# Optimization experiments

Measured on AMD Instinct MI355X. Metric: run time of the kernel, lower is better.

Reference implementation:

```python
import jax, jax.numpy as jnp
import numpy as np

L, D, V = 8, 1024, 32000
DT_MIN, DT_MAX = 0.01, 0.1
EPS = 1e-5


def _layer_norm(x, w, b):
    mu = jnp.mean(x, -1, keepdims=True)
    var = jnp.var(x, -1, keepdims=True)
    return (x - mu) * jax.lax.rsqrt(var + EPS) * w + b


def _encode(ids):
    # deterministic phase encoding of tokens onto the unit phase sphere
    theta = 2.0 * jnp.pi * ids.astype(jnp.float32) / V  # [B,S]
    k = jnp.arange(1, D // 2 + 1, dtype=jnp.float32)
    ang = theta[..., None] * k  # [B,S,D/2]
    return jnp.concatenate([jnp.cos(ang), jnp.sin(ang)], -1) / jnp.sqrt(jnp.float32(D))


def _flux(s, mask):
    # attention-like causal score from state self-interaction
    score = jnp.einsum('bqd,bkd->bqk', s, s) / jnp.sqrt(jnp.float32(D))
    score = jnp.where(mask, score, 0.0)
    return jnp.einsum('bqk,bkd->bqd', score, s), score


def _evolve_with_tunneling(s, dt, mask):
    # Heun-Euler (predictor-corrector) integration step
    k1, score = _flux(s, mask)
    mid = s + dt * k1
    k2, _ = _flux(mid, mask)
    ev = s + 0.5 * dt * (k1 + k2)
    # quantum tunneling: boost low-energy states proportionally to dt/dt_max
    energy = jnp.linalg.norm(ev, axis=-1)  # [B,S]
    thr = jnp.mean(energy, axis=-1, keepdims=True)
    tunnel = energy < thr
    strength = dt / DT_MAX  # [B,1,1]
    ev = jnp.where(tunnel[..., None], ev * (1.0 + strength), ev)
    ratio = jnp.mean(tunnel.astype(jnp.float32))
    return ev, score, ratio


def setup_inputs() -> dict:
    key = jax.random.key(0)
    ks = jax.random.split(key, 4)
    B, S = 2, 2048
    input_ids = jax.random.randint(ks[0], (B, S), 0, V)
    labels = jax.random.randint(ks[1], (B, S), 0, V)
    proj_w = jax.random.normal(ks[2], (L, D, D), jnp.float32) * 0.02
    proj_b = jnp.zeros((L, D), jnp.float32)
    ln_w = jnp.ones((L, D), jnp.float32)
    ln_b = jnp.zeros((L, D), jnp.float32)
    fln_w = jnp.ones((D,), jnp.float32)
    fln_b = jnp.zeros((D,), jnp.float32)
    out_w = jax.random.normal(ks[3], (D, V), jnp.float32) * 0.02
    return dict(input_ids=input_ids, labels=labels, proj_w=proj_w, proj_b=proj_b,
                ln_w=ln_w, ln_b=ln_b, fln_w=fln_w, fln_b=fln_b, out_w=out_w)


def reference(input_ids, labels, proj_w, proj_b, ln_w, ln_b, fln_w, fln_b, out_w):
    B, S = input_ids.shape
    mask = jnp.tril(jnp.ones((S, S), dtype=bool))
    # deterministic timestep (midpoint of [dt_min, dt_max]); dropout in eval mode
    dt = jnp.full((B, 1, 1), 0.5 * (DT_MIN + DT_MAX), jnp.float32)
    states = _encode(input_ids)
    for i in range(L):
        ev, _score, _ratio = _evolve_with_tunneling(states, dt, mask)
        states = _layer_norm(ev @ proj_w[i] + proj_b[i], ln_w[i], ln_b[i])
    states = _layer_norm(states, fln_w, fln_b)
    # normalized quantum projection to vocab
    energy = jnp.linalg.norm(states, axis=-1, keepdims=True)
    logits = (states / (energy + 1e-12)) @ out_w  # [B,S,V]
    # shifted cross-entropy
    sl = logits[:, :-1, :].reshape(-1, V)
    tl = labels[:, 1:].reshape(-1)
    logp = jax.nn.log_softmax(sl, axis=-1)
    loss = -jnp.mean(jnp.take_along_axis(logp, tl[:, None], axis=1))
    return logits, loss
```

## Files before the change

### kernel.cpp

```cpp
#include <hip/hip_runtime.h>

#define LL 8
#define DD 1024
#define VV 32000
#define SS 2048
#define BB 2
#define NROWS 4096
#define DT_STEP 0.055f
#define HALF_DT 0.0275f
#define TUNNEL_SCALE 1.55f

typedef __attribute__((ext_vector_type(8))) short bf16x8;
typedef __attribute__((ext_vector_type(4))) float f32x4;

static __device__ __forceinline__ float bf2f(unsigned short u){
  union { unsigned int i; float f; } v; v.i = ((unsigned int)u) << 16; return v.f;
}
static __device__ __forceinline__ unsigned short f2bf(float f){
  union { float f; unsigned int i; } v; v.f = f;
  unsigned int r = v.i + 0x7fffu + ((v.i >> 16) & 1u);
  return (unsigned short)(r >> 16);
}

static __device__ __forceinline__ void gl16(const unsigned short* g, unsigned short* l){
  __builtin_amdgcn_global_load_lds(
      (const __attribute__((address_space(1))) unsigned int*)g,
      (__attribute__((address_space(3))) unsigned int*)l, 16, 0, 0);
}

__device__ __forceinline__ float block_sum256(float v, volatile float* scratch){
  #pragma unroll
  for (int off = 32; off; off >>= 1) v += __shfl_down(v, off, 64);
  int w = threadIdx.x >> 6, lane = threadIdx.x & 63;
  __syncthreads();
  if (lane == 0) scratch[w] = v;
  __syncthreads();
  return scratch[0] + scratch[1] + scratch[2] + scratch[3];
}

__global__ void encode_kernel(const int* __restrict__ ids, float* __restrict__ s_f32,
                              unsigned short* __restrict__ hi, unsigned short* __restrict__ lo){
  int row = blockIdx.x;
  int t = threadIdx.x;
  float theta = 6.28318530717958647692f * (float)ids[row] / 32000.0f;
  #pragma unroll
  for (int i = 0; i < 2; ++i){
    int kk = t + i * 256;
    float ang = theta * (float)(kk + 1);
    float sv, cv; sincosf(ang, &sv, &cv);
    float c = cv * 0.03125f, s = sv * 0.03125f;
    long b0 = (long)row * DD + kk, b1 = b0 + 512;
    s_f32[b0] = c; s_f32[b1] = s;
    unsigned short ch = f2bf(c); hi[b0] = ch; lo[b0] = f2bf(c - bf2f(ch));
    unsigned short sh = f2bf(s); hi[b1] = sh; lo[b1] = f2bf(s - bf2f(sh));
  }
}

__global__ void transpose_bf16_pair_kernel(const unsigned short* __restrict__ in_hi,
                                           const unsigned short* __restrict__ in_lo,
                                           unsigned short* __restrict__ out_hi,
                                           unsigned short* __restrict__ out_lo,
                                           int R, int C){
  __shared__ __align__(16) unsigned short tile[64][80];
  int zz = blockIdx.z;
  const unsigned short* in = (zz & 1) ? in_lo : in_hi;
  unsigned short* out = (zz & 1) ? out_lo : out_hi;
  long ib = (long)(zz >> 1) * R * C;
  int c0 = blockIdx.x * 64, r0 = blockIdx.y * 64;
  int t = threadIdx.x;
  #pragma unroll
  for (int i = 0; i < 2; ++i){
    int j = t + i * 256; int row = j >> 3, cc = j & 7;
    *(uint4*)&tile[row][cc * 8] = *(const uint4*)(in + ib + (long)(r0 + row) * C + c0 + cc * 8);
  }
  __syncthreads();
  #pragma unroll
  for (int i = 0; i < 2; ++i){
    int j = t + i * 256; int orow = j >> 3, cc = j & 7;
    union { unsigned short u[8]; uint4 v; } tmp;
    #pragma unroll
    for (int e = 0; e < 8; ++e) tmp.u[e] = tile[cc * 8 + e][orow];
    *(uint4*)(out + ib + (long)(c0 + orow) * R + r0 + cc * 8) = tmp.v;
  }
}

template<bool SPLIT>
__global__ void transpose_f32_bf16_kernel(const float* __restrict__ in,
                                          unsigned short* __restrict__ ohi,
                                          unsigned short* __restrict__ olo, int R, int C){
  __shared__ float tile[64][68];
  long ib = (long)blockIdx.z * R * C;
  int c0 = blockIdx.x * 64, r0 = blockIdx.y * 64;
  int t = threadIdx.x;
  #pragma unroll
  for (int i = 0; i < 4; ++i){
    int j = t + i * 256; int row = j >> 4, cc = j & 15;
    *(float4*)&tile[row][cc * 4] = *(const float4*)(in + ib + (long)(r0 + row) * C + c0 + cc * 4);
  }
  __syncthreads();
  #pragma unroll
  for (int i = 0; i < 2; ++i){
    int j = t + i * 256; int orow = j >> 3, cc = j & 7;
    union { unsigned short u[8]; uint4 v; } th, tl;
    #pragma unroll
    for (int e = 0; e < 8; ++e){
      float v = tile[cc * 8 + e][orow];
      unsigned short h = f2bf(v); th.u[e] = h;
      if (SPLIT) tl.u[e] = f2bf(v - bf2f(h));
    }
    long ob = ib + (long)(c0 + orow) * R + r0 + cc * 8;
    *(uint4*)(ohi + ob) = th.v;
    if (SPLIT) *(uint4*)(olo + ob) = tl.v;
  }
}

template<int OUTMODE, int CAUSAL>
__global__ __launch_bounds__(512, 4)
void gemm_nt_kernel(const unsigned short* __restrict__ Ahi, const unsigned short* __restrict__ Alo,
                    const unsigned short* __restrict__ Bhi, const unsigned short* __restrict__ Blo,
                    float* __restrict__ C, unsigned short* __restrict__ Chi,
                    unsigned short* __restrict__ Clo, const float* __restrict__ bias,
                    const float* __restrict__ Sf, const float* __restrict__ K1f,
                    int K, int lda, int ldb, int ldc, int MT, int NT,
                    long batchA, long batchB, long batchC, float alpha)
{
  const int bz = blockIdx.y;
  const int nwg = MT * NT;
  const int q = nwg >> 3, r = nwg & 7;
  const int xcd = blockIdx.x & 7, off = blockIdx.x >> 3;
  const int wg = (xcd < r ? xcd * (q + 1) : r * (q + 1) + (xcd - r) * q) + off;
  const int band = wg / (NT << 3), rem = wg - band * (NT << 3);
  const int mt = (band << 3) + (rem & 7), nt = rem >> 3;
  if (CAUSAL == 1 && nt > mt) return;
  const int m0 = mt << 7, n0 = nt << 7;
  int Keff = K;
  if (CAUSAL == 2){ int kl = (mt + 1) << 7; Keff = kl < K ? kl : K; }

  __shared__ __align__(16) unsigned short sA[2][128][64];
  __shared__ __align__(16) unsigned short sB[2][128][64];

  const int tid = threadIdx.x;
  const int lane = tid & 63;
  const int w = tid >> 6;
  const int wr = w >> 2, wc = w & 3;
  const int fr = lane & 15, fc = lane >> 4;
  const int fr7 = fr & 7;

  f32x4 acc[4][2];
  #pragma unroll
  for (int i = 0; i < 4; ++i)
    #pragma unroll
    for (int j = 0; j < 2; ++j) acc[i][j] = (f32x4){0.f, 0.f, 0.f, 0.f};

  const int srow = tid >> 3, slot = tid & 7;
  const int cont = slot ^ (srow & 7);
  const long aoff = (long)bz * batchA, boff = (long)bz * batchB;
  const int gcol = (cont & 3) << 3;
  const unsigned short* gA = (cont >= 4 ? Alo : Ahi) + aoff + (long)(m0 + srow) * lda + gcol;
  const unsigned short* gB = (cont >= 4 ? Blo : Bhi) + boff + (long)(n0 + srow) * ldb + gcol;
  const long rstepA = 64L * lda, rstepB = 64L * ldb;
  const int wofs = w << 9;

  #define STAGE(buf, kt) do {                                        \
    gl16(gA + (kt),          &sA[buf][0][0] + wofs);                 \
    gl16(gA + (kt) + rstepA, &sA[buf][0][0] + 4096 + wofs);          \
    gl16(gB + (kt),          &sB[buf][0][0] + wofs);                 \
    gl16(gB + (kt) + rstepB, &sB[buf][0][0] + 4096 + wofs);          \
  } while(0)

  const int oh = (fc ^ fr7) << 4;
  const int ol = ((4 + fc) ^ fr7) << 4;

  #define COMPUTE(buf) do {                                                         \
    const char* bA_ = (const char*)&sA[buf][0][0];                                  \
    const char* bB_ = (const char*)&sB[buf][0][0];                                  \
    bf16x8 ah_[4], al_[4];                                                          \
    _Pragma("unroll")                                                               \
    for (int mi = 0; mi < 4; ++mi){                                                 \
      const char* p_ = bA_ + (wr * 64 + mi * 16 + fr) * 128;                        \
      ah_[mi] = *(const bf16x8*)(p_ + oh);                                          \
      al_[mi] = *(const bf16x8*)(p_ + ol);                                          \
    }                                                                               \
    _Pragma("unroll")                                                               \
    for (int ni = 0; ni < 2; ++ni){                                                 \
      const char* pb_ = bB_ + (wc * 32 + ni * 16 + fr) * 128;                       \
      bf16x8 bh_ = *(const bf16x8*)(pb_ + oh);                                      \
      bf16x8 bl_ = *(const bf16x8*)(pb_ + ol);                                      \
      _Pragma("unroll")                                                             \
      for (int mi = 0; mi < 4; ++mi){                                               \
        acc[mi][ni] = __builtin_amdgcn_mfma_f32_16x16x32_bf16(ah_[mi], bh_, acc[mi][ni], 0, 0, 0);\
        acc[mi][ni] = __builtin_amdgcn_mfma_f32_16x16x32_bf16(ah_[mi], bl_, acc[mi][ni], 0, 0, 0);\
        acc[mi][ni] = __builtin_amdgcn_mfma_f32_16x16x32_bf16(al_[mi], bh_, acc[mi][ni], 0, 0, 0);\
      }                                                                             \
    }                                                                               \
  } while(0)

  const int ntiles = Keff >> 5;

  STAGE(0, 0);
  int cur = 0;
  for (int t = 0; t < ntiles - 1; ++t){
    asm volatile("s_barrier" ::: "memory");
    STAGE(cur ^ 1, (t + 1) << 5);
    asm volatile("s_waitcnt vmcnt(4)" ::: "memory");
    asm volatile("s_barrier" ::: "memory");
    COMPUTE(cur);
    cur ^= 1;
  }
  asm volatile("s_waitcnt vmcnt(0)" ::: "memory");
  asm volatile("s_barrier" ::: "memory");
  COMPUTE(cur);

  #undef STAGE
  #undef COMPUTE

  const long coff = (long)bz * batchC;
  const int rb0 = m0 + wr * 64 + fc * 4;
  const int cb0 = n0 + wc * 32 + fr;
  #pragma unroll
  for (int mi = 0; mi < 4; ++mi){
    #pragma unroll
    for (int ni = 0; ni < 2; ++ni){
      #pragma unroll
      for (int rg = 0; rg < 4; ++rg){
        int row = rb0 + mi * 16 + rg;
        int col = cb0 + ni * 16;
        float v = acc[mi][ni][rg] * alpha;
        long idx = coff + (long)row * ldc + col;
        if (OUTMODE == 0){
          if (bias) v += bias[col];
          C[idx] = v;
        } else if (OUTMODE == 2){
          if (CAUSAL == 1 && col > row) v = 0.0f;
          unsigned short h = f2bf(v);
          Chi[idx] = h;
          Clo[idx] = f2bf(v - bf2f(h));
        } else if (OUTMODE == 3){
          C[idx] = v;
          float m = Sf[idx] + DT_STEP * v;
          unsigned short h = f2bf(m);
          Chi[idx] = h;
          Clo[idx] = f2bf(m - bf2f(h));
        } else {
          C[idx] = Sf[idx] + HALF_DT * (K1f[idx] + v);
        }
      }
    }
  }
}

__global__ __launch_bounds__(512, 2)
void gemm256_kernel(const unsigned short* __restrict__ A,
                    const unsigned short* __restrict__ Bt,
                    float* __restrict__ C)
{
  const int MT = 16, NT = 125;
  const int nwg = MT * NT;
  const int q = nwg >> 3, r = nwg & 7;
  const int xcd = blockIdx.x & 7, off = blockIdx.x >> 3;
  const int wg = (xcd < r ? xcd * (q + 1) : r * (q + 1) + (xcd - r) * q) + off;
  const int band = wg / (NT << 3), rem = wg - band * (NT << 3);
  const int mt = (band << 3) + (rem & 7), nt = rem >> 3;
  const int m0 = mt << 8, n0 = nt << 8;

  __shared__ __align__(16) unsigned short sA[2][256][64];
  __shared__ __align__(16) unsigned short sB[2][256][64];

  const int tid = threadIdx.x;
  const int lane = tid & 63;
  const int w = tid >> 6;
  const int wr = w >> 2, wc = w & 3;
  const int fr = lane & 15, fc = lane >> 4;
  const int fr7 = fr & 7;

  f32x4 acc[8][4];
  #pragma unroll
  for (int i = 0; i < 8; ++i)
    #pragma unroll
    for (int j = 0; j < 4; ++j) acc[i][j] = (f32x4){0.f, 0.f, 0.f, 0.f};

  const int srow = tid >> 3, slot = tid & 7;
  const int cont = slot ^ (srow & 7);
  const unsigned short* gA = A  + (long)(m0 + srow) * DD + (cont << 3);
  const unsigned short* gB = Bt + (long)(n0 + srow) * DD + (cont << 3);
  const int wofs = w << 9;

  #define SGA(buf, kt, i) gl16(gA + (long)((i) * 64) * DD + (kt), &sA[buf][0][0] + (i) * 4096 + wofs)
  #define SGB(buf, kt, i) gl16(gB + (long)((i) * 64) * DD + (kt), &sB[buf][0][0] + (i) * 4096 + wofs)

  const int oh = (fc ^ fr7) << 4;
  const int ol = ((4 + fc) ^ fr7) << 4;

  #pragma unroll
  for (int i = 0; i < 4; ++i){ SGA(0, 0, i); SGB(0, 0, i); }

  int cur = 0;
  for (int t = 0; t < 16; ++t){
    const int nk = (t + 1) << 6;
    const bool stg = (t < 15);
    const char* bA = (const char*)&sA[cur][0][0];
    const char* bB = (const char*)&sB[cur][0][0];
    bf16x8 aq[4][2], bq[4][2];

    if (stg){ SGA(cur ^ 1, nk, 0); SGA(cur ^ 1, nk, 1);
              asm volatile("s_waitcnt vmcnt(2)" ::: "memory"); }
    else    { asm volatile("s_waitcnt vmcnt(0)" ::: "memory"); }
    asm volatile("s_barrier" ::: "memory");
    #pragma unroll
    for (int mi = 0; mi < 4; ++mi){
      const char* p = bA + (wr * 128 + mi * 16 + fr) * 128;
      aq[mi][0] = *(const bf16x8*)(p + oh);
      aq[mi][1] = *(const bf16x8*)(p + ol);
    }
    #pragma unroll
    for (int ni = 0; ni < 2; ++ni){
      const char* p = bB + (wc * 64 + ni * 16 + fr) * 128;
      bq[ni][0] = *(const bf16x8*)(p + oh);
      bq[ni][1] = *(const bf16x8*)(p + ol);
    }
    __builtin_amdgcn_s_setprio(1);
    #pragma unroll
    for (int ks = 0; ks < 2; ++ks)
      #pragma unroll
      for (int mi = 0; mi < 4; ++mi)
        #pragma unroll
        for (int ni = 0; ni < 2; ++ni)
          acc[mi][ni] = __builtin_amdgcn_mfma_f32_16x16x32_bf16(aq[mi][ks], bq[ni][ks], acc[mi][ni], 0, 0, 0);
    __builtin_amdgcn_s_setprio(0);

    if (stg){ SGA(cur ^ 1, nk, 2); SGA(cur ^ 1, nk, 3); }
    asm volatile("s_barrier" ::: "memory");
    #pragma unroll
    for (int ni = 2; ni < 4; ++ni){
      const char* p = bB + (wc * 64 + ni * 16 + fr) * 128;
      bq[ni][0] = *(const bf16x8*)(p + oh);
      bq[ni][1] = *(const bf16x8*)(p + ol);
    }
    __builtin_amdgcn_s_setprio(1);
    #pragma unroll
    for (int ks = 0; ks < 2; ++ks)
      #pragma unroll
      for (int mi = 0; mi < 4; ++mi)
        #pragma unroll
        for (int ni = 2; ni < 4; ++ni)
          acc[mi][ni] = __builtin_amdgcn_mfma_f32_16x16x32_bf16(aq[mi][ks], bq[ni][ks], acc[mi][ni], 0, 0, 0);
    __builtin_amdgcn_s_setprio(0);

    if (stg){ SGB(cur ^ 1, nk, 0); SGB(cur ^ 1, nk, 1); }
    asm volatile("s_barrier" ::: "memory");
    #pragma unroll
    for (int mi = 0; mi < 4; ++mi){
      const char* p = bA + (wr * 128 + (mi + 4) * 16 + fr) * 128;
      aq[mi][0] = *(const bf16x8*)(p + oh);
      aq[mi][1] = *(const bf16x8*)(p + ol);
    }
    __builtin_amdgcn_s_setprio(1);
    #pragma unroll
    for (int ks = 0; ks < 2; ++ks)
      #pragma unroll
      for (int mi = 0; mi < 4; ++mi)
        #pragma unroll
        for (int ni = 2; ni < 4; ++ni)
          acc[mi + 4][ni] = __builtin_amdgcn_mfma_f32_16x16x32_bf16(aq[mi][ks], bq[ni][ks], acc[mi + 4][ni], 0, 0, 0);
    __builtin_amdgcn_s_setprio(0);

    if (stg){ SGB(cur ^ 1, nk, 2); SGB(cur ^ 1, nk, 3); }
    asm volatile("s_barrier" ::: "memory");
    __builtin_amdgcn_s_setprio(1);
    #pragma unroll
    for (int ks = 0; ks < 2; ++ks)
      #pragma unroll
      for (int mi = 0; mi < 4; ++mi)
        #pragma unroll
        for (int ni = 0; ni < 2; ++ni)
          acc[mi + 4][ni] = __builtin_amdgcn_mfma_f32_16x16x32_bf16(aq[mi][ks], bq[ni][ks], acc[mi + 4][ni], 0, 0, 0);
    __builtin_amdgcn_s_setprio(0);

    cur ^= 1;
  }
  #undef SGA
  #undef SGB

  const int rb0 = m0 + wr * 128 + fc * 4;
  const int cb0 = n0 + wc * 64 + fr;
  #pragma unroll
  for (int mi = 0; mi < 8; ++mi){
    #pragma unroll
    for (int ni = 0; ni < 4; ++ni){
      #pragma unroll
      for (int rg = 0; rg < 4; ++rg){
        int row = rb0 + mi * 16 + rg;
        int col = cb0 + ni * 16;
        C[(long)row * VV + col] = acc[mi][ni][rg];
      }
    }
  }
}

__global__ void energy_kernel(const float* __restrict__ ev, float* __restrict__ energy){
  int row = blockIdx.x, t = threadIdx.x;
  long base = (long)row * DD + t * 4;
  float4 v = *(const float4*)(ev + base);
  __shared__ float scratch[4];
  float n2 = block_sum256(v.x*v.x + v.y*v.y + v.z*v.z + v.w*v.w, scratch);
  if (t == 0) energy[row] = sqrtf(n2);
}

__global__ void mean_energy_kernel(const float* __restrict__ energy, float* __restrict__ thr){
  int b = blockIdx.x, t = threadIdx.x;
  float s = 0.f;
  for (int j = t; j < SS; j += 256) s += energy[b * SS + j];
  __shared__ float scratch[4];
  float tot = block_sum256(s, scratch);
  if (t == 0) thr[b] = tot * (1.0f / SS);
}

__global__ void tunnel_kernel(const float* __restrict__ ev, const float* __restrict__ energy,
                              const float* __restrict__ thr,
                              unsigned short* __restrict__ hi, unsigned short* __restrict__ lo){
  int row = blockIdx.x, t = threadIdx.x;
  float scale = (energy[row] < thr[row >> 11]) ? TUNNEL_SCALE : 1.0f;
  long base = (long)row * DD + t * 4;
  float4 v = *(const float4*)(ev + base);
  v.x *= scale; v.y *= scale; v.z *= scale; v.w *= scale;
  ushort4 hv, lv;
  hv.x = f2bf(v.x); lv.x = f2bf(v.x - bf2f(hv.x));
  hv.y = f2bf(v.y); lv.y = f2bf(v.y - bf2f(hv.y));
  hv.z = f2bf(v.z); lv.z = f2bf(v.z - bf2f(hv.z));
  hv.w = f2bf(v.w); lv.w = f2bf(v.w - bf2f(hv.w));
  *(ushort4*)(hi + base) = hv; *(ushort4*)(lo + base) = lv;
}

__global__ void ln_kernel(const float* __restrict__ h, const float* __restrict__ w,
                          const float* __restrict__ b, float* __restrict__ s_f32,
                          unsigned short* __restrict__ hi, unsigned short* __restrict__ lo){
  int row = blockIdx.x, t = threadIdx.x;
  long base = (long)row * DD + t * 4;
  float4 xv = *(const float4*)(h + base);
  __shared__ float scratch[4];
  float sum = block_sum256(xv.x + xv.y + xv.z + xv.w, scratch);
  float ssq = block_sum256(xv.x*xv.x + xv.y*xv.y + xv.z*xv.z + xv.w*xv.w, scratch);
  float mu = sum * (1.0f / DD);
  float var = ssq * (1.0f / DD) - mu * mu;
  float rstd = rsqrtf(var + 1e-5f);
  float4 wv = *(const float4*)(w + t * 4), bv = *(const float4*)(b + t * 4);
  float y0 = (xv.x - mu) * rstd * wv.x + bv.x;
  float y1 = (xv.y - mu) * rstd * wv.y + bv.y;
  float y2 = (xv.z - mu) * rstd * wv.z + bv.z;
  float y3 = (xv.w - mu) * rstd * wv.w + bv.w;
  float4 o; o.x = y0; o.y = y1; o.z = y2; o.w = y3;
  *(float4*)(s_f32 + base) = o;
  ushort4 hv, lv;
  hv.x = f2bf(y0); lv.x = f2bf(y0 - bf2f(hv.x));
  hv.y = f2bf(y1); lv.y = f2bf(y1 - bf2f(hv.y));
  hv.z = f2bf(y2); lv.z = f2bf(y2 - bf2f(hv.z));
  hv.w = f2bf(y3); lv.w = f2bf(y3 - bf2f(hv.w));
  *(ushort4*)(hi + base) = hv; *(ushort4*)(lo + base) = lv;
}

__global__ void fln_kernel(const float* __restrict__ s, const float* __restrict__ w,
                           const float* __restrict__ b, unsigned short* __restrict__ uhi){
  int row = blockIdx.x, t = threadIdx.x;
  long base = (long)row * DD + t * 4;
  float4 xv = *(const float4*)(s + base);
  __shared__ float scratch[4];
  float sum = block_sum256(xv.x + xv.y + xv.z + xv.w, scratch);
  float ssq = block_sum256(xv.x*xv.x + xv.y*xv.y + xv.z*xv.z + xv.w*xv.w, scratch);
  float mu = sum * (1.0f / DD);
  float var = ssq * (1.0f / DD) - mu * mu;
  float rstd = rsqrtf(var + 1e-5f);
  float4 wv = *(const float4*)(w + t * 4), bv = *(const float4*)(b + t * 4);
  float y0 = (xv.x - mu) * rstd * wv.x + bv.x;
  float y1 = (xv.y - mu) * rstd * wv.y + bv.y;
  float y2 = (xv.z - mu) * rstd * wv.z + bv.z;
  float y3 = (xv.w - mu) * rstd * wv.w + bv.w;
  float n2 = block_sum256(y0*y0 + y1*y1 + y2*y2 + y3*y3, scratch);
  float inv = 1.0f / (sqrtf(n2) + 1e-12f);
  ushort4 o;
  o.x = f2bf(y0 * inv); o.y = f2bf(y1 * inv);
  o.z = f2bf(y2 * inv); o.w = f2bf(y3 * inv);
  *(ushort4*)(uhi + base) = o;
}

__global__ void loss_rows_kernel(const float* __restrict__ logits, const int* __restrict__ labels,
                                 float* __restrict__ lrow){
  int idx = blockIdx.x;
  int b = idx / (SS - 1), q = idx - b * (SS - 1);
  const float* rowp = logits + (long)(b * SS + q) * VV;
  int t = threadIdx.x;
  float m = -1e30f, l = 0.f;
  for (int j = t; j < VV / 4; j += 256){
    float4 v = *(const float4*)(rowp + j * 4);
    float mv = fmaxf(fmaxf(v.x, v.y), fmaxf(v.z, v.w));
    if (mv > m){ l *= __expf(m - mv); m = mv; }
    l += __expf(v.x - m) + __expf(v.y - m) + __expf(v.z - m) + __expf(v.w - m);
  }
  __shared__ float sm[256], sl[256];
  sm[t] = m; sl[t] = l;
  __syncthreads();
  for (int off = 128; off; off >>= 1){
    if (t < off){
      float m2 = sm[t + off], l2 = sl[t + off];
      float M = fmaxf(sm[t], m2);
      sl[t] = sl[t] * __expf(sm[t] - M) + l2 * __expf(m2 - M);
      sm[t] = M;
    }
    __syncthreads();
  }
  if (t == 0){
    float lse = sm[0] + __logf(sl[0]);
    float tl = rowp[labels[b * SS + q + 1]];
    lrow[idx] = lse - tl;
  }
}

__global__ void loss_reduce_kernel(const float* __restrict__ lrow, float* __restrict__ dst){
  __shared__ float scratch[4];
  float s = 0.f;
  for (int j = threadIdx.x; j < BB * (SS - 1); j += 256) s += lrow[j];
  float tot = block_sum256(s, scratch);
  if (threadIdx.x == 0) dst[0] = tot / (float)(BB * (SS - 1));
}

extern "C" void kernel_launch(void* const* d_in, const int* in_sizes, int n_in,
                              void* d_out, int out_size, void* d_ws, size_t ws_size,
                              hipStream_t stream) {
  const int*   ids    = (const int*)d_in[0];
  const int*   labels = (const int*)d_in[1];
  const float* proj_w = (const float*)d_in[2];
  const float* proj_b = (const float*)d_in[3];
  const float* ln_w   = (const float*)d_in[4];
  const float* ln_b   = (const float*)d_in[5];
  const float* fln_w  = (const float*)d_in[6];
  const float* fln_b  = (const float*)d_in[7];
  const float* out_w  = (const float*)d_in[8];
  float* out = (float*)d_out;

  char* ws = (char*)d_ws;
  float*          s_f32 = (float*)(ws + 0);
  unsigned short* op_hi = (unsigned short*)(ws + 16777216);
  unsigned short* op_lo = (unsigned short*)(ws + 25165824);
  unsigned short* T_hi  = (unsigned short*)(ws + 33554432);
  unsigned short* T_lo  = (unsigned short*)(ws + 41943040);
  float*          k1    = (float*)(ws + 50331648);
  float*          k2    = (float*)(ws + 67108864);
  unsigned short* sc_hi = (unsigned short*)(ws + 83886080);
  unsigned short* sc_lo = (unsigned short*)(ws + 92274688);
  unsigned short* WhiT  = (unsigned short*)(ws + 100663296);
  unsigned short* WloT  = (unsigned short*)(ws + 117440512);
  float*          energy= (float*)(ws + 134217728);
  float*          thr   = (float*)(ws + 134234112);
  float*          lrow  = (float*)(ws + 134234368);
  unsigned short* owT   = T_hi;

  transpose_f32_bf16_kernel<true><<<dim3(16, 16, 8), 256, 0, stream>>>(proj_w, WhiT, WloT, DD, DD);
  encode_kernel<<<NROWS, 256, 0, stream>>>(ids, s_f32, op_hi, op_lo);
  transpose_bf16_pair_kernel<<<dim3(16, 32, 4), 256, 0, stream>>>(op_hi, op_lo, T_hi, T_lo, SS, DD);

  for (int l = 0; l < LL; ++l){
    gemm_nt_kernel<2, 1><<<dim3(256, 2), 512, 0, stream>>>(
        op_hi, op_lo, op_hi, op_lo, nullptr, sc_hi, sc_lo, nullptr, nullptr, nullptr,
        DD, DD, DD, SS, 16, 16, (long)SS * DD, (long)SS * DD, (long)SS * SS, 0.03125f);
    gemm_nt_kernel<3, 2><<<dim3(128, 2), 512, 0, stream>>>(
        sc_hi, sc_lo, T_hi, T_lo, k1, op_hi, op_lo, nullptr, s_f32, nullptr,
        SS, SS, SS, DD, 16, 8, (long)SS * SS, (long)DD * SS, (long)SS * DD, 1.0f);
    transpose_bf16_pair_kernel<<<dim3(16, 32, 4), 256, 0, stream>>>(op_hi, op_lo, T_hi, T_lo, SS, DD);
    gemm_nt_kernel<2, 1><<<dim3(256, 2), 512, 0, stream>>>(
        op_hi, op_lo, op_hi, op_lo, nullptr, sc_hi, sc_lo, nullptr, nullptr, nullptr,
        DD, DD, DD, SS, 16, 16, (long)SS * DD, (long)SS * DD, (long)SS * SS, 0.03125f);
    gemm_nt_kernel<4, 2><<<dim3(128, 2), 512, 0, stream>>>(
        sc_hi, sc_lo, T_hi, T_lo, k2, nullptr, nullptr, nullptr, s_f32, k1,
        SS, SS, SS, DD, 16, 8, (long)SS * SS, (long)DD * SS, (long)SS * DD, 1.0f);
    energy_kernel<<<NROWS, 256, 0, stream>>>(k2, energy);
    mean_energy_kernel<<<BB, 256, 0, stream>>>(energy, thr);
    tunnel_kernel<<<NROWS, 256, 0, stream>>>(k2, energy, thr, op_hi, op_lo);
    gemm_nt_kernel<0, 0><<<dim3(256, 1), 512, 0, stream>>>(
        op_hi, op_lo, WhiT + (long)l * DD * DD, WloT + (long)l * DD * DD,
        k1, nullptr, nullptr, proj_b + l * DD, nullptr, nullptr,
        DD, DD, DD, DD, 32, 8, 0, 0, 0, 1.0f);
    ln_kernel<<<NROWS, 256, 0, stream>>>(k1, ln_w + l * DD, ln_b + l * DD, s_f32, op_hi, op_lo);
    if (l < LL - 1){
      transpose_bf16_pair_kernel<<<dim3(16, 32, 4), 256, 0, stream>>>(op_hi, op_lo, T_hi, T_lo, SS, DD);
    }
  }

  transpose_f32_bf16_kernel<false><<<dim3(500, 16, 1), 256, 0, stream>>>(out_w, owT, nullptr, DD, VV);
  fln_kernel<<<NROWS, 256, 0, stream>>>(s_f32, fln_w, fln_b, op_hi);
  gemm256_kernel<<<2000, 512, 0, stream>>>(op_hi, owT, out);
  loss_rows_kernel<<<BB * (SS - 1), 256, 0, stream>>>(out, labels, lrow);
  loss_reduce_kernel<<<1, 256, 0, stream>>>(lrow, out + (long)NROWS * VV);
}
```

Baseline: 3.000 ms.

## Fuse partial log-sum-exp into vocab GEMM and deepen its K pipeline

The vocab projection GEMM now emits per-row partial max and sum-of-exp for each 64-column slice, so the loss kernel only reduces 500 partials per row instead of rereading the full 32000-wide logits row. Separately, the GEMM main loop is restructured from a double-buffered K=64 tile with split barrier phases into a 4-stage K=32 ring buffer with three tiles in flight. This removes a large second pass over the logits and aims to hide global-load latency better, in exchange for extra epilogue shuffles/exps and more barriers per K step. Partials are stored in workspace reused from the state buffer, which is no longer needed at that point.

```diff
diff --git a/kernel.cpp b/kernel.cpp
--- a/kernel.cpp
+++ b/kernel.cpp
@@ -252,7 +252,9 @@
 __global__ __launch_bounds__(512, 2)
 void gemm256_kernel(const unsigned short* __restrict__ A,
                     const unsigned short* __restrict__ Bt,
-                    float* __restrict__ C)
+                    float* __restrict__ C,
+                    float* __restrict__ pmax,
+                    float* __restrict__ psum)
 {
   const int MT = 16, NT = 125;
   const int nwg = MT * NT;
@@ -263,15 +265,14 @@
   const int mt = (band << 3) + (rem & 7), nt = rem >> 3;
   const int m0 = mt << 8, n0 = nt << 8;
 
-  __shared__ __align__(16) unsigned short sA[2][256][64];
-  __shared__ __align__(16) unsigned short sB[2][256][64];
+  __shared__ __align__(16) unsigned short sA[4][256][32];
+  __shared__ __align__(16) unsigned short sB[4][256][32];
 
   const int tid = threadIdx.x;
   const int lane = tid & 63;
   const int w = tid >> 6;
   const int wr = w >> 2, wc = w & 3;
   const int fr = lane & 15, fc = lane >> 4;
-  const int fr7 = fr & 7;
 
   f32x4 acc[8][4];
   #pragma unroll
@@ -279,107 +280,57 @@
     #pragma unroll
     for (int j = 0; j < 4; ++j) acc[i][j] = (f32x4){0.f, 0.f, 0.f, 0.f};
 
-  const int srow = tid >> 3, slot = tid & 7;
-  const int cont = slot ^ (srow & 7);
+  const int srow = tid >> 2, slot = tid & 3;
+  const int cont = slot ^ (srow & 3);
   const unsigned short* gA = A  + (long)(m0 + srow) * DD + (cont << 3);
   const unsigned short* gB = Bt + (long)(n0 + srow) * DD + (cont << 3);
   const int wofs = w << 9;
 
-  #define SGA(buf, kt, i) gl16(gA + (long)((i) * 64) * DD + (kt), &sA[buf][0][0] + (i) * 4096 + wofs)
-  #define SGB(buf, kt, i) gl16(gB + (long)((i) * 64) * DD + (kt), &sB[buf][0][0] + (i) * 4096 + wofs)
-
-  const int oh = (fc ^ fr7) << 4;
-  const int ol = ((4 + fc) ^ fr7) << 4;
-
-  #pragma unroll
-  for (int i = 0; i < 4; ++i){ SGA(0, 0, i); SGB(0, 0, i); }
-
-  int cur = 0;
-  for (int t = 0; t < 16; ++t){
-    const int nk = (t + 1) << 6;
-    const bool stg = (t < 15);
-    const char* bA = (const char*)&sA[cur][0][0];
-    const char* bB = (const char*)&sB[cur][0][0];
-    bf16x8 aq[4][2], bq[4][2];
-
-    if (stg){ SGA(cur ^ 1, nk, 0); SGA(cur ^ 1, nk, 1);
-              asm volatile("s_waitcnt vmcnt(2)" ::: "memory"); }
-    else    { asm volatile("s_waitcnt vmcnt(0)" ::: "memory"); }
+  #define STG(buf, kt) do {                                                  \
+    gl16(gA + (kt),                &sA[buf][0][0] + wofs);                   \
+    gl16(gA + 128L * DD + (kt),    &sA[buf][0][0] + 4096 + wofs);            \
+    gl16(gB + (kt),                &sB[buf][0][0] + wofs);                   \
+    gl16(gB + 128L * DD + (kt),    &sB[buf][0][0] + 4096 + wofs);            \
+  } while(0)
+
+  STG(0, 0); STG(1, 32); STG(2, 64);
+
+  for (int t = 0; t < 32; ++t){
     asm volatile("s_barrier" ::: "memory");
-    #pragma unroll
-    for (int mi = 0; mi < 4; ++mi){
-      const char* p = bA + (wr * 128 + mi * 16 + fr) * 128;
-      aq[mi][0] = *(const bf16x8*)(p + oh);
-      aq[mi][1] = *(const bf16x8*)(p + ol);
-    }
-    #pragma unroll
-    for (int ni = 0; ni < 2; ++ni){
-      const char* p = bB + (wc * 64 + ni * 16 + fr) * 128;
-      bq[ni][0] = *(const bf16x8*)(p + oh);
-      bq[ni][1] = *(const bf16x8*)(p + ol);
+    if (t < 29){
+      STG((t + 3) & 3, (t + 3) << 5);
+      asm volatile("s_waitcnt vmcnt(12)" ::: "memory");
+    } else if (t == 29){
+      asm volatile("s_waitcnt vmcnt(8)" ::: "memory");
+    } else if (t == 30){
+      asm volatile("s_waitcnt vmcnt(4)" ::: "memory");
+    } else {
+      asm volatile("s_waitcnt vmcnt(0)" ::: "memory");
+    }
+    asm volatile("s_barrier" ::: "memory");
+
+    const char* bA = (const char*)&sA[t & 3][0][0];
+    const char* bB = (const char*)&sB[t & 3][0][0];
+    bf16x8 aq[8], bq[4];
+    #pragma unroll
+    for (int mi = 0; mi < 8; ++mi){
+      const int row = wr * 128 + mi * 16 + fr;
+      aq[mi] = *(const bf16x8*)(bA + row * 64 + ((fc ^ (row & 3)) << 4));
+    }
+    #pragma unroll
+    for (int ni = 0; ni < 4; ++ni){
+      const int row = wc * 64 + ni * 16 + fr;
+      bq[ni] = *(const bf16x8*)(bB + row * 64 + ((fc ^ (row & 3)) << 4));
     }
     __builtin_amdgcn_s_setprio(1);
     #pragma unroll
-    for (int ks = 0; ks < 2; ++ks)
+    for (int mi = 0; mi < 8; ++mi)
       #pragma unroll
-      for (int mi = 0; mi < 4; ++mi)
-        #pragma unroll
-        for (int ni = 0; ni < 2; ++ni)
-          acc[mi][ni] = __builtin_amdgcn_mfma_f32_16x16x32_bf16(aq[mi][ks], bq[ni][ks], acc[mi][ni], 0, 0, 0);
+      for (int ni = 0; ni < 4; ++ni)
+        acc[mi][ni] = __builtin_amdgcn_mfma_f32_16x16x32_bf16(aq[mi], bq[ni], acc[mi][ni], 0, 0, 0);
     __builtin_amdgcn_s_setprio(0);
-
-    if (stg){ SGA(cur ^ 1, nk, 2); SGA(cur ^ 1, nk, 3); }
-    asm volatile("s_barrier" ::: "memory");
-    #pragma unroll
-    for (int ni = 2; ni < 4; ++ni){
-      const char* p = bB + (wc * 64 + ni * 16 + fr) * 128;
-      bq[ni][0] = *(const bf16x8*)(p + oh);
-      bq[ni][1] = *(const bf16x8*)(p + ol);
-    }
-    __builtin_amdgcn_s_setprio(1);
-    #pragma unroll
-    for (int ks = 0; ks < 2; ++ks)
-      #pragma unroll
-      for (int mi = 0; mi < 4; ++mi)
-        #pragma unroll
-        for (int ni = 2; ni < 4; ++ni)
-          acc[mi][ni] = __builtin_amdgcn_mfma_f32_16x16x32_bf16(aq[mi][ks], bq[ni][ks], acc[mi][ni], 0, 0, 0);
-    __builtin_amdgcn_s_setprio(0);
-
-    if (stg){ SGB(cur ^ 1, nk, 0); SGB(cur ^ 1, nk, 1); }
-    asm volatile("s_barrier" ::: "memory");
-    #pragma unroll
-    for (int mi = 0; mi < 4; ++mi){
-      const char* p = bA + (wr * 128 + (mi + 4) * 16 + fr) * 128;
-      aq[mi][0] = *(const bf16x8*)(p + oh);
-      aq[mi][1] = *(const bf16x8*)(p + ol);
-    }
-    __builtin_amdgcn_s_setprio(1);
-    #pragma unroll
-    for (int ks = 0; ks < 2; ++ks)
-      #pragma unroll
-      for (int mi = 0; mi < 4; ++mi)
-        #pragma unroll
-        for (int ni = 2; ni < 4; ++ni)
-          acc[mi + 4][ni] = __builtin_amdgcn_mfma_f32_16x16x32_bf16(aq[mi][ks], bq[ni][ks], acc[mi + 4][ni], 0, 0, 0);
-    __builtin_amdgcn_s_setprio(0);
-
-    if (stg){ SGB(cur ^ 1, nk, 2); SGB(cur ^ 1, nk, 3); }
-    asm volatile("s_barrier" ::: "memory");
-    __builtin_amdgcn_s_setprio(1);
-    #pragma unroll
-    for (int ks = 0; ks < 2; ++ks)
-      #pragma unroll
-      for (int mi = 0; mi < 4; ++mi)
-        #pragma unroll
-        for (int ni = 0; ni < 2; ++ni)
-          acc[mi + 4][ni] = __builtin_amdgcn_mfma_f32_16x16x32_bf16(aq[mi][ks], bq[ni][ks], acc[mi + 4][ni], 0, 0, 0);
-    __builtin_amdgcn_s_setprio(0);
-
-    cur ^= 1;
-  }
-  #undef SGA
-  #undef SGB
+  }
+  #undef STG
 
   const int rb0 = m0 + wr * 128 + fc * 4;
   const int cb0 = n0 + wc * 64 + fr;
@@ -389,9 +340,27 @@
     for (int ni = 0; ni < 4; ++ni){
       #pragma unroll
       for (int rg = 0; rg < 4; ++rg){
-        int row = rb0 + mi * 16 + rg;
-        int col = cb0 + ni * 16;
-        C[(long)row * VV + col] = acc[mi][ni][rg];
+        C[(long)(rb0 + mi * 16 + rg) * VV + cb0 + ni * 16] = acc[mi][ni][rg];
+      }
+    }
+  }
+
+  #pragma unroll
+  for (int mi = 0; mi < 8; ++mi){
+    #pragma unroll
+    for (int rg = 0; rg < 4; ++rg){
+      float m4 = fmaxf(fmaxf(acc[mi][0][rg], acc[mi][1][rg]),
+                       fmaxf(acc[mi][2][rg], acc[mi][3][rg]));
+      #pragma unroll
+      for (int o = 1; o < 16; o <<= 1) m4 = fmaxf(m4, __shfl_xor(m4, o, 64));
+      float s4 = __expf(acc[mi][0][rg] - m4) + __expf(acc[mi][1][rg] - m4)
+               + __expf(acc[mi][2][rg] - m4) + __expf(acc[mi][3][rg] - m4);
+      #pragma unroll
+      for (int o = 1; o < 16; o <<= 1) s4 += __shfl_xor(s4, o, 64);
+      if (fr == 0){
+        long pidx = ((long)(rb0 + mi * 16 + rg) << 9) + nt * 4 + wc;
+        pmax[pidx] = m4;
+        psum[pidx] = s4;
       }
     }
   }
@@ -482,34 +451,30 @@
   *(ushort4*)(uhi + base) = o;
 }
 
-__global__ void loss_rows_kernel(const float* __restrict__ logits, const int* __restrict__ labels,
-                                 float* __restrict__ lrow){
+__global__ void lse_reduce_kernel(const float* __restrict__ pmax, const float* __restrict__ psum,
+                                  const float* __restrict__ logits, const int* __restrict__ labels,
+                                  float* __restrict__ lrow){
   int idx = blockIdx.x;
-  int b = idx / (SS - 1), q = idx - b * (SS - 1);
-  const float* rowp = logits + (long)(b * SS + q) * VV;
+  int b = idx / (SS - 1), qq = idx - b * (SS - 1);
+  int row = b * SS + qq;
   int t = threadIdx.x;
   float m = -1e30f, l = 0.f;
-  for (int j = t; j < VV / 4; j += 256){
-    float4 v = *(const float4*)(rowp + j * 4);
-    float mv = fmaxf(fmaxf(v.x, v.y), fmaxf(v.z, v.w));
-    if (mv > m){ l *= __expf(m - mv); m = mv; }
-    l += __expf(v.x - m) + __expf(v.y - m) + __expf(v.z - m) + __expf(v.w - m);
-  }
-  __shared__ float sm[256], sl[256];
-  sm[t] = m; sl[t] = l;
-  __syncthreads();
-  for (int off = 128; off; off >>= 1){
-    if (t < off){
-      float m2 = sm[t + off], l2 = sl[t + off];
-      float M = fmaxf(sm[t], m2);
-      sl[t] = sl[t] * __expf(sm[t] - M) + l2 * __expf(m2 - M);
-      sm[t] = M;
-    }
-    __syncthreads();
+  for (int p = t; p < 500; p += 64){
+    float pm = pmax[((long)row << 9) + p], pl = psum[((long)row << 9) + p];
+    float M = fmaxf(m, pm);
+    l = l * __expf(m - M) + pl * __expf(pm - M);
+    m = M;
+  }
+  #pragma unroll
+  for (int o = 1; o < 64; o <<= 1){
+    float m2 = __shfl_xor(m, o, 64), l2 = __shfl_xor(l, o, 64);
+    float M = fmaxf(m, m2);
+    l = l * __expf(m - M) + l2 * __expf(m2 - M);
+    m = M;
   }
   if (t == 0){
-    float lse = sm[0] + __logf(sl[0]);
-    float tl = rowp[labels[b * SS + q + 1]];
+    float lse = m + __logf(l);
+    float tl = logits[(long)row * VV + labels[row + 1]];
     lrow[idx] = lse - tl;
   }
 }
@@ -552,6 +517,8 @@
   float*          thr   = (float*)(ws + 134234112);
   float*          lrow  = (float*)(ws + 134234368);
   unsigned short* owT   = T_hi;
+  float*          pmax  = (float*)(ws + 0);
+  float*          psum  = (float*)(ws + 8388608);
 
   transpose_f32_bf16_kernel<true><<<dim3(16, 16, 8), 256, 0, stream>>>(proj_w, WhiT, WloT, DD, DD);
   encode_kernel<<<NROWS, 256, 0, stream>>>(ids, s_f32, op_hi, op_lo);
@@ -586,7 +553,7 @@
 
   transpose_f32_bf16_kernel<false><<<dim3(500, 16, 1), 256, 0, stream>>>(out_w, owT, nullptr, DD, VV);
   fln_kernel<<<NROWS, 256, 0, stream>>>(s_f32, fln_w, fln_b, op_hi);
-  gemm256_kernel<<<2000, 512, 0, stream>>>(op_hi, owT, out);
-  loss_rows_kernel<<<BB * (SS - 1), 256, 0, stream>>>(out, labels, lrow);
+  gemm256_kernel<<<2000, 512, 0, stream>>>(op_hi, owT, out, pmax, psum);
+  lse_reduce_kernel<<<BB * (SS - 1), 64, 0, stream>>>(pmax, psum, out, labels, lrow);
   loss_reduce_kernel<<<1, 256, 0, stream>>>(lrow, out + (long)NROWS * VV);
 }
```

Measured after the change: 3.017 ms. About the same (+0.5%).

## Fuse softmax exp-sum partials into vocab GEMM epilogue, shrink loss kernel

Applied to the files above, without the earlier changes.

The vocab projection GEMM epilogue now computes per-row partial sums of exp(logit) over each wave's 64 columns and writes them to a workspace buffer. The loss kernel then sums 500 partials per row instead of rereading the full 32000-wide logits row, avoiding a large second pass over the logits. It drops the max subtraction, relying on the logits being small because the states are unit-normalized, and it reuses the s_f32 workspace region for the partials.

```diff
diff --git a/kernel.cpp b/kernel.cpp
--- a/kernel.cpp
+++ b/kernel.cpp
@@ -252,7 +252,8 @@
 __global__ __launch_bounds__(512, 2)
 void gemm256_kernel(const unsigned short* __restrict__ A,
                     const unsigned short* __restrict__ Bt,
-                    float* __restrict__ C)
+                    float* __restrict__ C,
+                    float* __restrict__ psum)
 {
   const int MT = 16, NT = 125;
   const int nwg = MT * NT;
@@ -389,9 +390,22 @@
     for (int ni = 0; ni < 4; ++ni){
       #pragma unroll
       for (int rg = 0; rg < 4; ++rg){
-        int row = rb0 + mi * 16 + rg;
-        int col = cb0 + ni * 16;
-        C[(long)row * VV + col] = acc[mi][ni][rg];
+        C[(long)(rb0 + mi * 16 + rg) * VV + cb0 + ni * 16] = acc[mi][ni][rg];
+      }
+    }
+  }
+
+  #pragma unroll
+  for (int mi = 0; mi < 8; ++mi){
+    #pragma unroll
+    for (int rg = 0; rg < 4; ++rg){
+      float s4 = __expf(acc[mi][0][rg]) + __expf(acc[mi][1][rg])
+               + __expf(acc[mi][2][rg]) + __expf(acc[mi][3][rg]);
+      #pragma unroll
+      for (int o = 1; o < 16; o <<= 1) s4 += __shfl_xor(s4, o, 64);
+      if (fr == 0){
+        long pidx = ((long)(rb0 + mi * 16 + rg) << 9) + nt * 4 + wc;
+        psum[pidx] = s4;
       }
     }
   }
@@ -482,34 +496,20 @@
   *(ushort4*)(uhi + base) = o;
 }
 
-__global__ void loss_rows_kernel(const float* __restrict__ logits, const int* __restrict__ labels,
-                                 float* __restrict__ lrow){
+__global__ void lse_reduce_kernel(const float* __restrict__ psum,
+                                  const float* __restrict__ logits, const int* __restrict__ labels,
+                                  float* __restrict__ lrow){
   int idx = blockIdx.x;
-  int b = idx / (SS - 1), q = idx - b * (SS - 1);
-  const float* rowp = logits + (long)(b * SS + q) * VV;
+  int b = idx / (SS - 1), qq = idx - b * (SS - 1);
+  int row = b * SS + qq;
   int t = threadIdx.x;
-  float m = -1e30f, l = 0.f;
-  for (int j = t; j < VV / 4; j += 256){
-    float4 v = *(const float4*)(rowp + j * 4);
-    float mv = fmaxf(fmaxf(v.x, v.y), fmaxf(v.z, v.w));
-    if (mv > m){ l *= __expf(m - mv); m = mv; }
-    l += __expf(v.x - m) + __expf(v.y - m) + __expf(v.z - m) + __expf(v.w - m);
-  }
-  __shared__ float sm[256], sl[256];
-  sm[t] = m; sl[t] = l;
-  __syncthreads();
-  for (int off = 128; off; off >>= 1){
-    if (t < off){
-      float m2 = sm[t + off], l2 = sl[t + off];
-      float M = fmaxf(sm[t], m2);
-      sl[t] = sl[t] * __expf(sm[t] - M) + l2 * __expf(m2 - M);
-      sm[t] = M;
-    }
-    __syncthreads();
-  }
+  float l = 0.f;
+  for (int p = t; p < 500; p += 64) l += psum[((long)row << 9) + p];
+  #pragma unroll
+  for (int o = 1; o < 64; o <<= 1) l += __shfl_xor(l, o, 64);
   if (t == 0){
-    float lse = sm[0] + __logf(sl[0]);
-    float tl = rowp[labels[b * SS + q + 1]];
+    float lse = __logf(l);
+    float tl = logits[(long)row * VV + labels[row + 1]];
     lrow[idx] = lse - tl;
   }
 }
@@ -552,6 +552,7 @@
   float*          thr   = (float*)(ws + 134234112);
   float*          lrow  = (float*)(ws + 134234368);
   unsigned short* owT   = T_hi;
+  float*          psum  = (float*)(ws + 0);
 
   transpose_f32_bf16_kernel<true><<<dim3(16, 16, 8), 256, 0, stream>>>(proj_w, WhiT, WloT, DD, DD);
   encode_kernel<<<NROWS, 256, 0, stream>>>(ids, s_f32, op_hi, op_lo);
@@ -586,7 +587,7 @@
 
   transpose_f32_bf16_kernel<false><<<dim3(500, 16, 1), 256, 0, stream>>>(out_w, owT, nullptr, DD, VV);
   fln_kernel<<<NROWS, 256, 0, stream>>>(s_f32, fln_w, fln_b, op_hi);
-  gemm256_kernel<<<2000, 512, 0, stream>>>(op_hi, owT, out);
-  loss_rows_kernel<<<BB * (SS - 1), 256, 0, stream>>>(out, labels, lrow);
+  gemm256_kernel<<<2000, 512, 0, stream>>>(op_hi, owT, out, psum);
+  lse_reduce_kernel<<<BB * (SS - 1), 64, 0, stream>>>(psum, out, labels, lrow);
   loss_reduce_kernel<<<1, 256, 0, stream>>>(lrow, out + (long)NROWS * VV);
 }
```

Result: faster. 2.939 ms (-2.0%).
